# Kernel optimization log

Measured on AMD Instinct MI355X. Metric: run time of the kernel, lower is better.

The kernel has to match this reference:

```python
import jax, jax.numpy as jnp
import numpy as np

NA, NP_, E = 40000, 60000, 80000
D, H = 512, 8
DK = D // H
SQRT_DK = float(DK) ** 0.5


def setup_inputs() -> dict:
    key = jax.random.key(0)
    ks = list(jax.random.split(key, 20))
    it = iter(ks)

    def nrm(shape, scale=1.0):
        return jax.random.normal(next(it), shape, dtype=jnp.float32) * scale

    xav = (6.0 / (DK + DK)) ** 0.5  # xavier_uniform bound for (dk, dk)
    w_scale = D ** -0.5
    inp = {
        "h_author": nrm((NA, D)),
        "h_paper": nrm((NP_, D)),
        "writes_src": jax.random.randint(next(it), (E,), 0, NA, dtype=jnp.int32),
        "writes_dst": jax.random.randint(next(it), (E,), 0, NP_, dtype=jnp.int32),
        "cites_src": jax.random.randint(next(it), (E,), 0, NP_, dtype=jnp.int32),
        "cites_dst": jax.random.randint(next(it), (E,), 0, NP_, dtype=jnp.int32),
        "wb_src": jax.random.randint(next(it), (E,), 0, NP_, dtype=jnp.int32),
        "wb_dst": jax.random.randint(next(it), (E,), 0, NA, dtype=jnp.int32),
        # per-node-type linear weights (2 types: 0=author, 1=paper)
        "Wk": nrm((2, D, D), w_scale), "bk": jnp.zeros((2, D), jnp.float32),
        "Wq": nrm((2, D, D), w_scale), "bq": jnp.zeros((2, D), jnp.float32),
        "Wv": nrm((2, D, D), w_scale), "bv": jnp.zeros((2, D), jnp.float32),
        "Wa": nrm((2, D, D), w_scale), "ba": jnp.zeros((2, D), jnp.float32),
        # per-relation params (3 relations: 0=writes, 1=cites, 2=written_by)
        "rel_att": jax.random.uniform(next(it), (3, H, DK, DK), jnp.float32, -xav, xav),
        "rel_msg": jax.random.uniform(next(it), (3, H, DK, DK), jnp.float32, -xav, xav),
        "rel_pri": jnp.ones((3, H), jnp.float32),
        "skip": jnp.ones((2,), jnp.float32),
    }
    return inp


def _edge_attn_agg(k, q, v, src, dst, pri, n_dst):
    # k, v: (N_src, H, DK) relation-transformed; q: (N_dst, H, DK)
    s = jnp.einsum('ehd,ehd->eh', q[dst], k[src]) * pri / SQRT_DK  # (E, H)
    m = jax.ops.segment_max(s, dst, num_segments=n_dst)            # edge softmax by dst
    ex = jnp.exp(s - m[dst])
    den = jax.ops.segment_sum(ex, dst, num_segments=n_dst)
    a = ex / den[dst]
    return jax.ops.segment_sum(v[src] * a[:, :, None], dst, num_segments=n_dst)


def reference(h_author, h_paper, writes_src, writes_dst, cites_src, cites_dst,
              wb_src, wb_dst, Wk, bk, Wq, bq, Wv, bv, Wa, ba,
              rel_att, rel_msg, rel_pri, skip):
    def proj(h, W, b, t):
        return (h @ W[t] + b[t]).reshape(-1, H, DK)

    k_a, v_a, q_a = proj(h_author, Wk, bk, 0), proj(h_author, Wv, bv, 0), proj(h_author, Wq, bq, 0)
    k_p, v_p, q_p = proj(h_paper, Wk, bk, 1), proj(h_paper, Wv, bv, 1), proj(h_paper, Wq, bq, 1)

    def rel(k, v, r):
        return (jnp.einsum('nhd,hde->nhe', k, rel_att[r]),
                jnp.einsum('nhd,hde->nhe', v, rel_msg[r]))

    k0, v0 = rel(k_a, v_a, 0)  # writes: author -> paper
    agg_w = _edge_attn_agg(k0, q_p, v0, writes_src, writes_dst, rel_pri[0], NP_)
    k1, v1 = rel(k_p, v_p, 1)  # cites: paper -> paper
    agg_c = _edge_attn_agg(k1, q_p, v1, cites_src, cites_dst, rel_pri[1], NP_)
    k2, v2 = rel(k_p, v_p, 2)  # written_by: paper -> author
    agg_b = _edge_attn_agg(k2, q_a, v2, wb_src, wb_dst, rel_pri[2], NA)

    t_paper = ((agg_w + agg_c) * 0.5).reshape(NP_, D)  # cross_reducer='mean'
    t_author = agg_b.reshape(NA, D)

    alpha = jax.nn.sigmoid(skip)
    out_a = (t_author @ Wa[0] + ba[0]) * alpha[0] + h_author * (1.0 - alpha[0])
    out_p = (t_paper @ Wa[1] + ba[1]) * alpha[1] + h_paper * (1.0 - alpha[1])
    return out_a, out_p
```

## Files before the change

### kernel.cpp

```cpp
#include <hip/hip_runtime.h>
#include <math.h>

#define D_ 512
#define H_ 8

typedef short bf16x8 __attribute__((ext_vector_type(8)));
typedef float f32x4 __attribute__((ext_vector_type(4)));

__device__ __forceinline__ unsigned short f2bf(float x) {
  unsigned int u = __float_as_uint(x);
  unsigned int r = (u + 0x7fff + ((u >> 16) & 1)) >> 16;
  return (unsigned short)r;
}
__device__ __forceinline__ float bf2f(unsigned short b) {
  return __uint_as_float(((unsigned int)b) << 16);
}

__device__ __forceinline__ long pk_idx(int n, int k) {
  int nt = n >> 7, njj = (n >> 4) & 7, rl = n & 15;
  int kt = k >> 6, kk = (k >> 5) & 1, q = (k >> 3) & 3, e = k & 7;
  return ((((long)(nt * 8 + kt) * 2 + kk) * 8 + njj) * 64 + (q * 16 + rl)) * 8 + e;
}

struct PrepArgs {
  const float *hA, *hP;
  unsigned short *hA16, *hP16;
  const float *fWin[6], *fbin[6], *frel[6];
  unsigned short *fpk[6];
  int fnoff[6];
  float *fbf[6];
  const float *tW[4];
  unsigned short *tpk[4];
  const float *cin[2];
  float *cout[2];
  int *degree;
  int NT;
  int b1, b2, b3, b4, b5;
};

__global__ __launch_bounds__(512) void prep_kernel(PrepArgs p) {
  const int b = blockIdx.x, t = threadIdx.x;
  if (b < p.b2) {
    const float* in; unsigned short* out; long i;
    if (b < p.b1) { in = p.hA; out = p.hA16; i = (long)b * 512 + t; }
    else          { in = p.hP; out = p.hP16; i = (long)(b - p.b1) * 512 + t; }
    float4 a = ((const float4*)in)[i * 2];
    float4 c = ((const float4*)in)[i * 2 + 1];
    bf16x8 o;
    o[0] = (short)f2bf(a.x); o[1] = (short)f2bf(a.y);
    o[2] = (short)f2bf(a.z); o[3] = (short)f2bf(a.w);
    o[4] = (short)f2bf(c.x); o[5] = (short)f2bf(c.y);
    o[6] = (short)f2bf(c.z); o[7] = (short)f2bf(c.w);
    ((bf16x8*)out)[i] = o;
  } else if (b < p.b3) {
    int idx = b - p.b2;
    int job = idx / 513, row = idx - job * 513;
    int h = t >> 6, e = t & 63;
    const float* src = (row < D_) ? (p.fWin[job] + (long)row * D_) : p.fbin[job];
    const float* rl = p.frel[job] + h * 64 * 64;
    float acc = 0.f;
#pragma unroll 16
    for (int d = 0; d < 64; ++d)
      acc = fmaf(src[h * 64 + d], rl[d * 64 + e], acc);
    if (row < D_) p.fpk[job][pk_idx(p.fnoff[job] + t, row)] = f2bf(acc);
    else p.fbf[job][t] = acc;
  } else if (b < p.b4) {
    int idx = b - p.b3;
    int job = idx >> 9, n = idx & 511;
    p.tpk[job][pk_idx(n, t)] = f2bf(p.tW[job][(long)t * D_ + n]);
  } else if (b < p.b5) {
    int job = b - p.b4;
    p.cout[job][t] = p.cin[job][t];
  } else {
    int i = (b - p.b5) * 512 + t;
    if (i < p.NT) p.degree[i] = 0;
  }
}

__global__ void hist_kernel(const int* __restrict__ w_dst,
                            const int* __restrict__ c_dst,
                            const int* __restrict__ b_dst,
                            int* __restrict__ degree, int E, int NP) {
  int i = blockIdx.x * blockDim.x + threadIdx.x;
  if (i >= 3 * E) return;
  int r = i / E, e = i - r * E;
  int d, base;
  if (r == 0)      { d = w_dst[e]; base = 0; }
  else if (r == 1) { d = c_dst[e]; base = NP; }
  else             { d = b_dst[e]; base = 2 * NP; }
  atomicAdd(degree + base + d, 1);
}

__global__ void scan1_kernel(const int* __restrict__ in, int* __restrict__ out,
                             int* __restrict__ aux, int n) {
  __shared__ int tmp[256];
  int t = threadIdx.x;
  int i = blockIdx.x * 256 + t;
  int v = (i < n) ? in[i] : 0;
  tmp[t] = v;
  __syncthreads();
#pragma unroll
  for (int d = 1; d < 256; d <<= 1) {
    int add = (t >= d) ? tmp[t - d] : 0;
    __syncthreads();
    tmp[t] += add;
    __syncthreads();
  }
  if (i < n) out[i] = tmp[t] - v;
  if (t == 255) aux[blockIdx.x] = tmp[255];
}

__global__ void scan2_kernel(int* __restrict__ aux, int nb) {
  __shared__ int tmp[1024];
  int t = threadIdx.x;
  int v = (t < nb) ? aux[t] : 0;
  tmp[t] = v;
  __syncthreads();
#pragma unroll
  for (int d = 1; d < 1024; d <<= 1) {
    int add = (t >= d) ? tmp[t - d] : 0;
    __syncthreads();
    tmp[t] += add;
    __syncthreads();
  }
  if (t < nb) aux[t] = tmp[t] - v;
}

__global__ void scan3_kernel(int* __restrict__ starts, int* __restrict__ cursor,
                             const int* __restrict__ aux, int n) {
  int i = blockIdx.x * 256 + threadIdx.x;
  if (i >= n) return;
  int s = starts[i] + aux[blockIdx.x];
  starts[i] = s;
  cursor[i] = s;
}

__global__ void scatter_kernel(const int* __restrict__ w_src, const int* __restrict__ w_dst,
                               const int* __restrict__ c_src, const int* __restrict__ c_dst,
                               const int* __restrict__ b_src, const int* __restrict__ b_dst,
                               int* __restrict__ cursor, int* __restrict__ csr,
                               int E, int NP) {
  int i = blockIdx.x * blockDim.x + threadIdx.x;
  if (i >= 3 * E) return;
  int r = i / E, e = i - r * E;
  int s, d, base;
  if (r == 0)      { s = w_src[e]; d = w_dst[e]; base = 0; }
  else if (r == 1) { s = c_src[e]; d = c_dst[e]; base = NP; }
  else             { s = b_src[e]; d = b_dst[e]; base = 2 * NP; }
  int pos = atomicAdd(cursor + base + d, 1);
  csr[pos] = s;
}

__global__ __launch_bounds__(256) void attn_all(
    const unsigned short* __restrict__ Pq,
    const unsigned short* __restrict__ Akw, const unsigned short* __restrict__ Avw,
    const unsigned short* __restrict__ Pkc, const unsigned short* __restrict__ Pvc,
    const unsigned short* __restrict__ Aq,
    const unsigned short* __restrict__ Pkb, const unsigned short* __restrict__ Pvb,
    const int* __restrict__ csr, const int* __restrict__ starts,
    const int* __restrict__ degree, const float* __restrict__ pri,
    unsigned short* __restrict__ t16, int NP, int NA, int NAp) {
  long gid = (long)blockIdx.x * blockDim.x + threadIdx.x;
  int gw = (int)(gid >> 6);
  if (gw >= NP + NAp) return;
  int lane = threadIdx.x & 63;
  int h = lane >> 3, off = (lane & 7) << 3;

  const unsigned short* q;
  long orow;
  int node;
  const int paper = gw < NP;
  if (paper) {
    node = gw; q = Pq;
    orow = (long)(NAp + node) * D_ + h * 64 + off;
  } else {
    int aw = gw - NP;
    orow = (long)aw * D_ + h * 64 + off;
    if (aw >= NA) {
      bf16x8 z;
#pragma unroll
      for (int r = 0; r < 8; ++r) z[r] = 0;
      *(bf16x8*)(t16 + orow) = z;
      return;
    }
    node = aw; q = Aq;
  }

  bf16x8 qv = *(const bf16x8*)(q + (long)node * D_ + h * 64 + off);
  float qf[8];
#pragma unroll
  for (int r = 0; r < 8; ++r) qf[r] = bf2f((unsigned short)qv[r]);

  float res[8] = {};

  auto process = [&](const unsigned short* K, const unsigned short* V,
                     int nodeabs, float ps) {
    int st = starts[nodeabs], dg = degree[nodeabs];
    float m = -INFINITY, l = 0.f;
    float acc[8] = {};
    for (int i = 0; i < dg; ++i) {
      int s = csr[st + i];
      const long ro = (long)s * D_ + h * 64 + off;
      bf16x8 kv = *(const bf16x8*)(K + ro);
      bf16x8 vv = *(const bf16x8*)(V + ro);
      float dot = 0.f;
#pragma unroll
      for (int r = 0; r < 8; ++r)
        dot = fmaf(qf[r], bf2f((unsigned short)kv[r]), dot);
      dot += __shfl_xor(dot, 1);
      dot += __shfl_xor(dot, 2);
      dot += __shfl_xor(dot, 4);
      float sc = dot * ps;
      float mn = fmaxf(m, sc);
      float scale = __expf(m - mn);
      float pv = __expf(sc - mn);
      l = l * scale + pv;
#pragma unroll
      for (int r = 0; r < 8; ++r)
        acc[r] = acc[r] * scale + pv * bf2f((unsigned short)vv[r]);
      m = mn;
    }
    if (l > 0.f) {
      float inv = 1.f / l;
#pragma unroll
      for (int r = 0; r < 8; ++r) res[r] += acc[r] * inv;
    }
  };

  float outscale;
  if (paper) {
    process(Akw, Avw, node, pri[h] * 0.125f);
    process(Pkc, Pvc, NP + node, pri[8 + h] * 0.125f);
    outscale = 0.5f;
  } else {
    process(Pkb, Pvb, 2 * NP + node, pri[16 + h] * 0.125f);
    outscale = 1.0f;
  }

  bf16x8 o;
#pragma unroll
  for (int r = 0; r < 8; ++r) o[r] = (short)f2bf(res[r] * outscale);
  *(bf16x8*)(t16 + orow) = o;
}

__device__ __forceinline__ void gload_lds16(const void* g, void* l) {
  __builtin_amdgcn_global_load_lds(
      (const __attribute__((address_space(1))) void*)g,
      (__attribute__((address_space(3))) void*)l, 16, 0, 0);
}

#define GEMM_CORE(A_PTR, PK_PTR)                                              \
  f32x4 acc[4][4] = {};                                                       \
  const int rr = lane & 15;                                                   \
  const int qk = lane >> 4;                                                   \
  const int rx = (rr & 7) << 4;                                               \
  auto STAGE_A = [&](int slot, int tile) {                                    \
    const int k0 = tile * 64 + swz;                                           \
    _Pragma("unroll")                                                         \
    for (int j = 0; j < 4; ++j) {                                             \
      int gr = bm + srow + j * 32;                                            \
      if (gr >= M) gr = M - 1;                                                \
      gload_lds16((A_PTR) + (long)gr * D_ + k0,                               \
                  &As[slot][j * 2048 + wave * 512]);                          \
    }                                                                         \
  };                                                                          \
  STAGE_A(0, 0); STAGE_A(1, 1);                                               \
  _Pragma("unroll")                                                           \
  for (int t = 0; t < 8; ++t) {                                               \
    asm volatile("s_waitcnt vmcnt(4)" ::: "memory");                          \
    __builtin_amdgcn_s_barrier();                                             \
    asm volatile("" ::: "memory");                                            \
    bf16x8 bfr[8];                                                            \
    _Pragma("unroll")                                                         \
    for (int kk = 0; kk < 2; ++kk)                                            \
      _Pragma("unroll")                                                       \
      for (int nj = 0; nj < 4; ++nj)                                          \
        bfr[kk * 4 + nj] = *(const bf16x8*)((PK_PTR) +                        \
            ((long)((nt * 8 + t) * 16 + kk * 8 + (wn >> 4) + nj) * 64 +       \
             lane) * 8);                                                      \
    bf16x8 af[8];                                                             \
    const char* ab = (const char*)&As[t % 3][0];                              \
    _Pragma("unroll")                                                         \
    for (int kk = 0; kk < 2; ++kk) {                                          \
      const int cs = (kk * 64 + qk * 16) ^ rx;                                \
      _Pragma("unroll")                                                       \
      for (int mi = 0; mi < 4; ++mi)                                          \
        af[kk * 4 + mi] =                                                     \
            *(const bf16x8*)(ab + (wm + mi * 16 + rr) * 128 + cs);            \
    }                                                                         \
    if (t + 2 < 8) STAGE_A((t + 2) % 3, t + 2);                               \
    __builtin_amdgcn_s_setprio(1);                                            \
    _Pragma("unroll")                                                         \
    for (int kk = 0; kk < 2; ++kk)                                            \
      _Pragma("unroll")                                                       \
      for (int mi = 0; mi < 4; ++mi)                                          \
        _Pragma("unroll")                                                     \
        for (int nj = 0; nj < 4; ++nj)                                        \
          acc[mi][nj] = __builtin_amdgcn_mfma_f32_16x16x32_bf16(              \
              af[kk * 4 + mi], bfr[kk * 4 + nj], acc[mi][nj], 0, 0, 0);       \
    __builtin_amdgcn_s_setprio(0);                                            \
    asm volatile("" ::: "memory");                                            \
  }

struct ProjArgs {
  const unsigned short *A0, *A1;
  const unsigned short *PK0, *PK1;
  const float *bias0, *bias1;
  void* outs[8];
  int M0, M1, split;
};

struct OutArgs {
  const unsigned short* A;
  const unsigned short *PK0, *PK1;
  const float *bias0, *bias1;
  const float *H0, *H1;
  const float* skip;
  float *o0, *o1;
  int mtsplit, NAp, M0, M1;
};

__global__ __launch_bounds__(256, 3) void gemm_proj(ProjArgs pa) {
  __shared__ unsigned short As[3][128 * 64];

  const int nwg = gridDim.x, orig = blockIdx.x;
  const int q8 = nwg >> 3, r8 = nwg & 7;
  const int xcd = orig & 7, pos = orig >> 3;
  const int wgid =
      (xcd < r8 ? xcd * (q8 + 1) : r8 * (q8 + 1) + (xcd - r8) * q8) + pos;

  int reg, mt, nt;
  if (wgid < pa.split) { reg = 0; mt = wgid / 12; nt = wgid - mt * 12; }
  else { int r = wgid - pa.split; reg = 1; mt = r / 20; nt = r - mt * 20; }
  const unsigned short* A  = reg ? pa.A1 : pa.A0;
  const unsigned short* PK = reg ? pa.PK1 : pa.PK0;
  const float* bias = reg ? pa.bias1 : pa.bias0;
  const int M = reg ? pa.M1 : pa.M0;
  const int bm = mt * 128, bn = nt * 128;

  const int tid = threadIdx.x;
  const int wave = tid >> 6, lane = tid & 63;
  const int wm = (wave >> 1) * 64;
  const int wn = (wave & 1) * 64;
  const int srow = tid >> 3;
  const int swz = ((tid & 7) ^ (srow & 7)) * 8;

  GEMM_CORE(A, PK)

  const int cr = (lane >> 4) * 4;
  const int cc = lane & 15;
  const int matu = (bn + wn) >> 9;
  const int wcb = (bn + wn) & 511;
  unsigned short* ob16 = (unsigned short*)pa.outs[(reg ? 3 : 0) + matu];
#pragma unroll
  for (int mi = 0; mi < 4; ++mi) {
    int rowb = bm + wm + mi * 16 + cr;
#pragma unroll
    for (int nj = 0; nj < 4; ++nj) {
      float bb = bias[bn + wn + nj * 16 + cc];
#pragma unroll
      for (int r = 0; r < 4; ++r) {
        int row = rowb + r;
        if (row >= M) continue;
        ob16[(long)row * D_ + wcb + nj * 16 + cc] = f2bf(acc[mi][nj][r] + bb);
      }
    }
  }
}

__global__ __launch_bounds__(256, 3) void gemm_out(OutArgs oa) {
  __shared__ unsigned short As[3][128 * 64];

  const int nwg = gridDim.x, orig = blockIdx.x;
  const int q8 = nwg >> 3, r8 = nwg & 7;
  const int xcd = orig & 7, pos = orig >> 3;
  const int wgid =
      (xcd < r8 ? xcd * (q8 + 1) : r8 * (q8 + 1) + (xcd - r8) * q8) + pos;

  const int bmt = wgid >> 2;
  const int nt = wgid & 3;
  const int bn = nt * 128;
  const int reg = bmt >= oa.mtsplit;
  const int bm = (reg ? bmt - oa.mtsplit : bmt) * 128;
  const int abase = reg ? oa.NAp : 0;
  const int M = reg ? oa.M1 : oa.M0;
  const unsigned short* A  = oa.A + (long)abase * D_;
  const unsigned short* PK = reg ? oa.PK1 : oa.PK0;
  const float* bias = reg ? oa.bias1 : oa.bias0;
  const float* Hres = reg ? oa.H1 : oa.H0;
  float* outp = reg ? oa.o1 : oa.o0;

  const int tid = threadIdx.x;
  const int wave = tid >> 6, lane = tid & 63;
  const int wm = (wave >> 1) * 64;
  const int wn = (wave & 1) * 64;
  const int srow = tid >> 3;
  const int swz = ((tid & 7) ^ (srow & 7)) * 8;

  GEMM_CORE(A, PK)

  float sv = oa.skip[reg];
  float alpha = 1.f / (1.f + expf(-sv));
  float beta = 1.f - alpha;
  const int cr = (lane >> 4) * 4;
  const int cc = lane & 15;
#pragma unroll
  for (int mi = 0; mi < 4; ++mi) {
    int rowb = bm + wm + mi * 16 + cr;
#pragma unroll
    for (int nj = 0; nj < 4; ++nj) {
      int col = bn + wn + nj * 16 + cc;
      float bb = bias[col];
#pragma unroll
      for (int r = 0; r < 4; ++r) {
        int row = rowb + r;
        if (row >= M) continue;
        float val = acc[mi][nj][r] + bb;
        val = val * alpha + Hres[(long)row * D_ + col] * beta;
        outp[(long)row * D_ + col] = val;
      }
    }
  }
}

extern "C" void kernel_launch(void* const* d_in, const int* in_sizes, int n_in,
                              void* d_out, int out_size, void* d_ws, size_t ws_size,
                              hipStream_t stream) {
  const float* h_author = (const float*)d_in[0];
  const float* h_paper  = (const float*)d_in[1];
  const int* w_src = (const int*)d_in[2];
  const int* w_dst = (const int*)d_in[3];
  const int* c_src = (const int*)d_in[4];
  const int* c_dst = (const int*)d_in[5];
  const int* b_src = (const int*)d_in[6];
  const int* b_dst = (const int*)d_in[7];
  const float* Wk = (const float*)d_in[8];
  const float* bk = (const float*)d_in[9];
  const float* Wq = (const float*)d_in[10];
  const float* bq = (const float*)d_in[11];
  const float* Wv = (const float*)d_in[12];
  const float* bv = (const float*)d_in[13];
  const float* Wa = (const float*)d_in[14];
  const float* ba = (const float*)d_in[15];
  const float* rel_att = (const float*)d_in[16];
  const float* rel_msg = (const float*)d_in[17];
  const float* rel_pri = (const float*)d_in[18];
  const float* skip = (const float*)d_in[19];

  const int NA = in_sizes[0] / D_;
  const int NP = in_sizes[1] / D_;
  const int E  = in_sizes[2];
  const int NT = 2 * NP + NA;
  const int tA = (NA + 127) / 128;
  const int tP = (NP + 127) / 128;
  const int NAp = tA * 128;

  char* w = (char*)d_ws;
  auto alloc = [&](long bytes) {
    char* p = w;
    w += (bytes + 255) & ~255L;
    return p;
  };
  unsigned short* hA16 = (unsigned short*)alloc((long)NA * D_ * 2);
  unsigned short* hP16 = (unsigned short*)alloc((long)NP * D_ * 2);
  unsigned short* Pq   = (unsigned short*)alloc((long)NP * D_ * 2);
  unsigned short* Pkc  = (unsigned short*)alloc((long)NP * D_ * 2);
  unsigned short* Pvc  = (unsigned short*)alloc((long)NP * D_ * 2);
  unsigned short* Pkb  = (unsigned short*)alloc((long)NP * D_ * 2);
  unsigned short* Pvb  = (unsigned short*)alloc((long)NP * D_ * 2);
  unsigned short* Aq   = (unsigned short*)alloc((long)NA * D_ * 2);
  unsigned short* Akw  = (unsigned short*)alloc((long)NA * D_ * 2);
  unsigned short* Avw  = (unsigned short*)alloc((long)NA * D_ * 2);
  unsigned short* t16  = (unsigned short*)alloc((long)(NAp + NP) * D_ * 2);
  unsigned short* PKP  = (unsigned short*)alloc((long)2560 * D_ * 2);
  unsigned short* PKA  = (unsigned short*)alloc((long)1536 * D_ * 2);
  float* bfP           = (float*)alloc(2560 * 4);
  float* bfA           = (float*)alloc(1536 * 4);
  unsigned short* PK0  = (unsigned short*)alloc((long)D_ * D_ * 2);
  unsigned short* PK1  = (unsigned short*)alloc((long)D_ * D_ * 2);
  int* degree          = (int*)alloc((long)NT * 4);
  int* starts          = (int*)alloc((long)NT * 4);
  int* cursor          = (int*)alloc((long)NT * 4);
  int* csr             = (int*)alloc((long)3 * E * 4);
  int* aux             = (int*)alloc(((long)NT / 256 + 2) * 4);

  const long WD = (long)D_ * D_;
  const long RS = (long)H_ * 64 * 64;

  float* out_a = (float*)d_out;
  float* out_p = out_a + (long)NA * D_;

  {
    PrepArgs p;
    p.hA = h_author; p.hP = h_paper; p.hA16 = hA16; p.hP16 = hP16;
    p.fWin[0] = Wk + WD; p.fbin[0] = bk + D_; p.frel[0] = rel_att + RS;
    p.fpk[0] = PKP; p.fnoff[0] = 512;  p.fbf[0] = bfP + 512;
    p.fWin[1] = Wv + WD; p.fbin[1] = bv + D_; p.frel[1] = rel_msg + RS;
    p.fpk[1] = PKP; p.fnoff[1] = 1024; p.fbf[1] = bfP + 1024;
    p.fWin[2] = Wk + WD; p.fbin[2] = bk + D_; p.frel[2] = rel_att + 2 * RS;
    p.fpk[2] = PKP; p.fnoff[2] = 1536; p.fbf[2] = bfP + 1536;
    p.fWin[3] = Wv + WD; p.fbin[3] = bv + D_; p.frel[3] = rel_msg + 2 * RS;
    p.fpk[3] = PKP; p.fnoff[3] = 2048; p.fbf[3] = bfP + 2048;
    p.fWin[4] = Wk;      p.fbin[4] = bk;      p.frel[4] = rel_att;
    p.fpk[4] = PKA; p.fnoff[4] = 512;  p.fbf[4] = bfA + 512;
    p.fWin[5] = Wv;      p.fbin[5] = bv;      p.frel[5] = rel_msg;
    p.fpk[5] = PKA; p.fnoff[5] = 1024; p.fbf[5] = bfA + 1024;
    p.tW[0] = Wq + WD; p.tpk[0] = PKP;
    p.tW[1] = Wq;      p.tpk[1] = PKA;
    p.tW[2] = Wa;      p.tpk[2] = PK0;
    p.tW[3] = Wa + WD; p.tpk[3] = PK1;
    p.cin[0] = bq + D_; p.cout[0] = bfP;
    p.cin[1] = bq;      p.cout[1] = bfA;
    p.degree = degree; p.NT = NT;
    p.b1 = NA / 8;
    p.b2 = p.b1 + NP / 8;
    p.b3 = p.b2 + 6 * 513;
    p.b4 = p.b3 + 4 * 512;
    p.b5 = p.b4 + 2;
    int total = p.b5 + (NT + 511) / 512;
    prep_kernel<<<total, 512, 0, stream>>>(p);
  }

  {
    int th = 3 * E;
    hist_kernel<<<(th + 255) / 256, 256, 0, stream>>>(w_dst, c_dst, b_dst,
                                                      degree, E, NP);
    int nb = (NT + 255) / 256;
    scan1_kernel<<<nb, 256, 0, stream>>>(degree, starts, aux, NT);
    scan2_kernel<<<1, 1024, 0, stream>>>(aux, nb);
    scan3_kernel<<<nb, 256, 0, stream>>>(starts, cursor, aux, NT);
    scatter_kernel<<<(th + 255) / 256, 256, 0, stream>>>(
        w_src, w_dst, c_src, c_dst, b_src, b_dst, cursor, csr, E, NP);
  }

  {
    ProjArgs pa;
    pa.A0 = hA16; pa.A1 = hP16;
    pa.PK0 = PKA; pa.PK1 = PKP;
    pa.bias0 = bfA; pa.bias1 = bfP;
    pa.outs[0] = Aq;  pa.outs[1] = Akw; pa.outs[2] = Avw;
    pa.outs[3] = Pq;  pa.outs[4] = Pkc; pa.outs[5] = Pvc;
    pa.outs[6] = Pkb; pa.outs[7] = Pvb;
    pa.M0 = NA; pa.M1 = NP;
    pa.split = tA * 12;
    int nwg = pa.split + tP * 20;
    gemm_proj<<<nwg, 256, 0, stream>>>(pa);
  }

  {
    long th = (long)(NP + NAp) * 64;
    attn_all<<<(int)((th + 255) / 256), 256, 0, stream>>>(
        Pq, Akw, Avw, Pkc, Pvc, Aq, Pkb, Pvb,
        csr, starts, degree, rel_pri, t16, NP, NA, NAp);
  }

  {
    OutArgs oa;
    oa.A = t16;
    oa.PK0 = PK0; oa.PK1 = PK1;
    oa.bias0 = ba; oa.bias1 = ba + D_;
    oa.H0 = h_author; oa.H1 = h_paper;
    oa.skip = skip;
    oa.o0 = out_a; oa.o1 = out_p;
    oa.mtsplit = tA; oa.NAp = NAp; oa.M0 = NA; oa.M1 = NP;
    int nwg = (tA + tP) * 4;
    gemm_out<<<nwg, 256, 0, stream>>>(oa);
  }
}
```

Baseline: 885.5 us.

## Double-buffer GEMM B-fragment loads and shortcut degree-one softmax nodes

The GEMM core now prefetches the packed weight fragments for the next K-tile into alternating register buffers, so their global loads overlap the current tile's MFMAs. The vmcnt waits are adjusted to match the larger number of loads in flight. Separately, the edge attention path skips the dot product and exp for nodes with exactly one incoming edge, since the softmax weight there is 1. The prefetch raises register pressure, which could reduce occupancy, and the hand-tuned waitcnt values must match the load counts exactly or stale data will be read.

New measurement: 876.4 us. Within noise of the previous version (-1.0%).

```diff
diff --git a/kernel.cpp b/kernel.cpp
--- a/kernel.cpp
+++ b/kernel.cpp
@@ -196,6 +196,13 @@
   auto process = [&](const unsigned short* K, const unsigned short* V,
                      int nodeabs, float ps) {
     int st = starts[nodeabs], dg = degree[nodeabs];
+    if (dg == 1) {
+      int s = csr[st];
+      bf16x8 vv = *(const bf16x8*)(V + (long)s * D_ + h * 64 + off);
+#pragma unroll
+      for (int r = 0; r < 8; ++r) res[r] += bf2f((unsigned short)vv[r]);
+      return;
+    }
     float m = -INFINITY, l = 0.f;
     float acc[8] = {};
     for (int i = 0; i < dg; ++i) {
@@ -249,11 +256,40 @@
       (__attribute__((address_space(3))) void*)l, 16, 0, 0);
 }
 
+#define LOAD_B_(dst, tile)                                                    \
+  _Pragma("unroll")                                                           \
+  for (int kk = 0; kk < 2; ++kk)                                              \
+    _Pragma("unroll")                                                         \
+    for (int nj = 0; nj < 4; ++nj)                                            \
+      dst[kk * 4 + nj] = *(const bf16x8*)(PKp +                               \
+          ((long)((nt * 8 + (tile)) * 16 + kk * 8 + (wn >> 4) + nj) * 64 +    \
+           lane) * 8);
+
+#define MFMA_T(bc, ab)                                                        \
+  __builtin_amdgcn_s_setprio(1);                                              \
+  _Pragma("unroll")                                                           \
+  for (int kk = 0; kk < 2; ++kk) {                                            \
+    const int cs = (kk * 64 + qk * 16) ^ rx;                                  \
+    bf16x8 af[4];                                                             \
+    _Pragma("unroll")                                                         \
+    for (int mi = 0; mi < 4; ++mi)                                            \
+      af[mi] = *(const bf16x8*)((ab) + (wm + mi * 16 + rr) * 128 + cs);       \
+    _Pragma("unroll")                                                         \
+    for (int mi = 0; mi < 4; ++mi)                                            \
+      _Pragma("unroll")                                                       \
+      for (int nj = 0; nj < 4; ++nj)                                          \
+        acc[mi][nj] = __builtin_amdgcn_mfma_f32_16x16x32_bf16(                \
+            af[mi], (bc)[kk * 4 + nj], acc[mi][nj], 0, 0, 0);                 \
+  }                                                                           \
+  __builtin_amdgcn_s_setprio(0);
+
 #define GEMM_CORE(A_PTR, PK_PTR)                                              \
   f32x4 acc[4][4] = {};                                                       \
+  const unsigned short* PKp = (PK_PTR);                                       \
   const int rr = lane & 15;                                                   \
   const int qk = lane >> 4;                                                   \
   const int rx = (rr & 7) << 4;                                               \
+  bf16x8 bA[8], bB[8];                                                        \
   auto STAGE_A = [&](int slot, int tile) {                                    \
     const int k0 = tile * 64 + swz;                                           \
     _Pragma("unroll")                                                         \
@@ -264,41 +300,21 @@
                   &As[slot][j * 2048 + wave * 512]);                          \
     }                                                                         \
   };                                                                          \
+  LOAD_B_(bA, 0)                                                              \
   STAGE_A(0, 0); STAGE_A(1, 1);                                               \
   _Pragma("unroll")                                                           \
   for (int t = 0; t < 8; ++t) {                                               \
-    asm volatile("s_waitcnt vmcnt(4)" ::: "memory");                          \
+    if (t == 0)     asm volatile("s_waitcnt vmcnt(4)" ::: "memory");          \
+    else if (t < 7) asm volatile("s_waitcnt vmcnt(12)" ::: "memory");         \
+    else            asm volatile("s_waitcnt vmcnt(8)" ::: "memory");          \
     __builtin_amdgcn_s_barrier();                                             \
     asm volatile("" ::: "memory");                                            \
-    bf16x8 bfr[8];                                                            \
-    _Pragma("unroll")                                                         \
-    for (int kk = 0; kk < 2; ++kk)                                            \
-      _Pragma("unroll")                                                       \
-      for (int nj = 0; nj < 4; ++nj)                                          \
-        bfr[kk * 4 + nj] = *(const bf16x8*)((PK_PTR) +                        \
-            ((long)((nt * 8 + t) * 16 + kk * 8 + (wn >> 4) + nj) * 64 +       \
-             lane) * 8);                                                      \
-    bf16x8 af[8];                                                             \
+    if ((t & 1) == 0) { if (t + 1 < 8) { LOAD_B_(bB, t + 1) } }               \
+    else              { if (t + 1 < 8) { LOAD_B_(bA, t + 1) } }               \
+    asm volatile("" ::: "memory");                                            \
     const char* ab = (const char*)&As[t % 3][0];                              \
-    _Pragma("unroll")                                                         \
-    for (int kk = 0; kk < 2; ++kk) {                                          \
-      const int cs = (kk * 64 + qk * 16) ^ rx;                                \
-      _Pragma("unroll")                                                       \
-      for (int mi = 0; mi < 4; ++mi)                                          \
-        af[kk * 4 + mi] =                                                     \
-            *(const bf16x8*)(ab + (wm + mi * 16 + rr) * 128 + cs);            \
-    }                                                                         \
     if (t + 2 < 8) STAGE_A((t + 2) % 3, t + 2);                               \
-    __builtin_amdgcn_s_setprio(1);                                            \
-    _Pragma("unroll")                                                         \
-    for (int kk = 0; kk < 2; ++kk)                                            \
-      _Pragma("unroll")                                                       \
-      for (int mi = 0; mi < 4; ++mi)                                          \
-        _Pragma("unroll")                                                     \
-        for (int nj = 0; nj < 4; ++nj)                                        \
-          acc[mi][nj] = __builtin_amdgcn_mfma_f32_16x16x32_bf16(              \
-              af[kk * 4 + mi], bfr[kk * 4 + nj], acc[mi][nj], 0, 0, 0);       \
-    __builtin_amdgcn_s_setprio(0);                                            \
+    if ((t & 1) == 0) { MFMA_T(bA, ab) } else { MFMA_T(bB, ab) }              \
     asm volatile("" ::: "memory");                                            \
   }
 
```
